# Optimization experiments

Hardware: AMD Instinct MI355X
Metric: run time of the kernel (lower is better)

The kernel has to match this reference:

```python
import jax, jax.numpy as jnp
import numpy as np

N_NODES = 100000
N_EDGES = 1600000
D = 128


def setup_inputs() -> dict:
    key = jax.random.key(0)
    ks = jax.random.split(key, 10)
    features = jax.random.normal(ks[0], (N_NODES, D), dtype=jnp.float32)
    edge_index = jax.random.randint(ks[1], (2, N_EDGES), 0, N_NODES, dtype=jnp.int64)
    edge_weight = jax.random.uniform(ks[2], (N_EDGES,), dtype=jnp.float32)
    scale = 1.0 / np.sqrt(D)
    W1 = jax.random.normal(ks[3], (D, D), dtype=jnp.float32) * scale
    b1 = jnp.zeros((D,), dtype=jnp.float32)
    a1 = jnp.full((D,), 0.25, dtype=jnp.float32)  # PReLU init
    W2 = jax.random.normal(ks[4], (D, D), dtype=jnp.float32) * scale
    b2 = jnp.zeros((D,), dtype=jnp.float32)
    a2 = jnp.full((D,), 0.25, dtype=jnp.float32)
    return {"features": features, "edge_index": edge_index, "edge_weight": edge_weight,
            "W1": W1, "b1": b1, "a1": a1, "W2": W2, "b2": b2, "a2": a2}


def _gcn_norm(edge_index, edge_weight, n_nodes):
    # PyG GCNConv default: add self-loops (weight 1), symmetric normalization.
    src, dst = edge_index[0], edge_index[1]
    loop = jnp.arange(n_nodes, dtype=src.dtype)
    src = jnp.concatenate([src, loop])
    dst = jnp.concatenate([dst, loop])
    w = jnp.concatenate([edge_weight, jnp.ones((n_nodes,), edge_weight.dtype)])
    deg = jax.ops.segment_sum(w, dst, num_segments=n_nodes)  # in-degree (target)
    dis = jnp.where(deg > 0, jax.lax.rsqrt(deg), 0.0)
    norm = dis[src] * w * dis[dst]  # [E + N]
    return src, dst, norm


def _gcn_layer(x, W, b, src, dst, norm, n_nodes):
    h = x @ W                                 # [N, D] dense GEMM first (PyG order)
    msg = h[src] * norm[:, None]              # gather + scale, [E+N, D]
    out = jax.ops.segment_sum(msg, dst, num_segments=n_nodes)
    return out + b


def _prelu(x, a):
    return jnp.where(x >= 0, x, a * x)


def reference(features, edge_index, edge_weight, W1, b1, a1, W2, b2, a2):
    n = features.shape[0]
    src, dst, norm = _gcn_norm(edge_index, edge_weight, n)
    # dropout is identity in eval mode
    x = _prelu(_gcn_layer(features, W1, b1, src, dst, norm, n), a1)
    x = _prelu(_gcn_layer(x, W2, b2, src, dst, norm, n), a2)
    return x
```

## Files before the change

### kernel.cpp

```cpp
#include <hip/hip_runtime.h>
#include <cstdint>

#define NN 100000
#define NE 1600000
#define DD 128
#define NB 250
#define BSZ 400

typedef unsigned int uint;
typedef unsigned short ushort;
typedef unsigned long long u64;

typedef __attribute__((ext_vector_type(8))) short short8;
typedef __attribute__((ext_vector_type(4))) float floatx4;

__device__ inline uint f2bf(float f) {
    uint u = __float_as_uint(f);
    return (u + 0x7fffu + ((u >> 16) & 1u)) >> 16;
}


__global__ __launch_bounds__(256) void zero_bc(uint* __restrict__ bc) {
    if (threadIdx.x < NB) bc[threadIdx.x] = 0u;
}

__global__ __launch_bounds__(256) void bucket_hist(const int* __restrict__ dst,
                                                   uint* __restrict__ bc) {
    __shared__ uint h[NB];
    int tid = threadIdx.x;
    if (tid < NB) h[tid] = 0u;
    __syncthreads();
    int e0 = blockIdx.x * 8192 + tid;
#pragma unroll
    for (int k = 0; k < 32; ++k) {
        int e = e0 + 256 * k;
        if (e < NE) atomicAdd(&h[(uint)dst[e] / BSZ], 1u);
    }
    __syncthreads();
    if (tid < NB && h[tid]) atomicAdd(&bc[tid], h[tid]);
}

__global__ __launch_bounds__(256) void bucket_prefix(const uint* __restrict__ bc,
                                                     uint* __restrict__ bbase,
                                                     uint* __restrict__ bcur) {
    int lane = threadIdx.x;
    if (lane < 64) {
        uint v[4], s = 0;
#pragma unroll
        for (int k = 0; k < 4; ++k) {
            int i = lane * 4 + k;
            v[k] = (i < NB) ? bc[i] : 0u;
            s += v[k];
        }
        uint inc = s;
#pragma unroll
        for (int d = 1; d < 64; d <<= 1) {
            uint t = __shfl_up(inc, (unsigned)d, 64);
            if (lane >= d) inc += t;
        }
        uint run = inc - s;
#pragma unroll
        for (int k = 0; k < 4; ++k) {
            int i = lane * 4 + k;
            if (i < NB) { bbase[i] = run; bcur[i] = run; run += v[k]; }
        }
        if (lane == 63) bbase[NB] = run;
    }
}

__global__ __launch_bounds__(256) void bucket_append(const int* __restrict__ src,
                                                     const int* __restrict__ dst,
                                                     const float* __restrict__ w,
                                                     uint* __restrict__ bcur,
                                                     int2* __restrict__ etmp) {
    __shared__ uint h[NB];
    __shared__ uint res[NB];
    int tid = threadIdx.x;
    if (tid < NB) h[tid] = 0u;
    __syncthreads();
    int e0 = blockIdx.x * 4096 + tid;
    uint rank[16], bkt[16];
#pragma unroll
    for (int k = 0; k < 16; ++k) {
        int e = e0 + 256 * k;
        if (e < NE) {
            uint b = (uint)dst[e] / BSZ;
            bkt[k] = b;
            rank[k] = atomicAdd(&h[b], 1u);
        } else bkt[k] = 0xffffffffu;
    }
    __syncthreads();
    if (tid < NB) res[tid] = h[tid] ? atomicAdd(&bcur[tid], h[tid]) : 0u;
    __syncthreads();
#pragma unroll
    for (int k = 0; k < 16; ++k) {
        if (bkt[k] != 0xffffffffu) {
            int e = e0 + 256 * k;
            uint dl = (uint)dst[e] - bkt[k] * BSZ;
            uint wq = (uint)(w[e] * 8388608.0f);
            if (wq > 8388607u) wq = 8388607u;
            etmp[res[bkt[k]] + rank[k]] = make_int2(src[e], (int)((dl << 23) | wq));
        }
    }
}

__global__ __launch_bounds__(256) void bucket_build(const int2* __restrict__ etmp,
                                                    const uint* __restrict__ bbase,
                                                    float* __restrict__ dis,
                                                    int* __restrict__ hist_g,
                                                    int* __restrict__ rowstart,
                                                    int2* __restrict__ edges) {
    __shared__ u64   wc[BSZ];
    __shared__ uint  cur[BSZ];
    __shared__ float disl[BSZ];
    int tid = threadIdx.x;
    int b = blockIdx.x;
    int n0 = b * BSZ;
    for (int i = tid; i < BSZ; i += 256) wc[i] = 0ull;
    __syncthreads();
    uint base = bbase[b], end = bbase[b + 1];
    for (uint i = base + tid; i < end; i += 256) {
        uint y = (uint)etmp[i].y;
        uint dl = y >> 23;
        atomicAdd(&wc[dl], ((u64)1 << 40) | (u64)(y & 0x7fffffu));
    }
    __syncthreads();
    if (tid < 64) {
        uint v[7], s = 0;
#pragma unroll
        for (int k = 0; k < 7; ++k) {
            int i = tid * 7 + k;
            v[k] = (i < BSZ) ? (uint)(wc[i] >> 40) : 0u;
            s += v[k];
        }
        uint inc = s;
#pragma unroll
        for (int d = 1; d < 64; d <<= 1) {
            uint t = __shfl_up(inc, (unsigned)d, 64);
            if (tid >= d) inc += t;
        }
        uint run = inc - s;
#pragma unroll
        for (int k = 0; k < 7; ++k) {
            int i = tid * 7 + k;
            if (i < BSZ) { cur[i] = run; run += v[k]; }
        }
    }
    __syncthreads();
    for (int i = tid; i < BSZ; i += 256) {
        u64 v = wc[i];
        float wsum = (float)(v & 0xffffffffffull) * (1.0f / 8388608.0f);
        float ds = rsqrtf(1.0f + wsum);
        disl[i] = ds;
        dis[n0 + i] = ds;
        hist_g[n0 + i] = (int)(v >> 40);
        rowstart[n0 + i] = (int)(base + cur[i]);
    }
    __syncthreads();
    for (uint i = base + tid; i < end; i += 256) {
        int2 e = etmp[i];
        uint y = (uint)e.y;
        uint dl = y >> 23;
        float wv = (float)(y & 0x7fffffu) * (1.0f / 8388608.0f);
        uint p = atomicAdd(&cur[dl], 1u);
        float nrm = wv * disl[dl];
        edges[base + p] = make_int2(e.x, __float_as_int(nrm));
    }
}

#define WTS 136
#define NTILES ((NN + 63) / 64)

template <bool AF32>
__global__ __launch_bounds__(256) void gemm_mfma(const void* __restrict__ Xv,
                                                 const float* __restrict__ W,
                                                 const float* __restrict__ dis,
                                                 ushort* __restrict__ HB) {
    __shared__ ushort Wt[DD * WTS];
    int tid = threadIdx.x;
#pragma unroll
    for (int it = 0; it < 16; ++it) {
        int flat = (tid + it * 256) * 4;
        int k = flat >> 7, n = flat & 127;
        float4 wv = *(const float4*)&W[flat];
        Wt[(n + 0) * WTS + k] = (ushort)f2bf(wv.x);
        Wt[(n + 1) * WTS + k] = (ushort)f2bf(wv.y);
        Wt[(n + 2) * WTS + k] = (ushort)f2bf(wv.z);
        Wt[(n + 3) * WTS + k] = (ushort)f2bf(wv.w);
    }
    __syncthreads();

    int wave = tid >> 6, lane = tid & 63;
    int q = lane >> 4, l16 = lane & 15;

    for (int tile = blockIdx.x; tile < NTILES; tile += gridDim.x) {
        int row0 = tile * 64 + wave * 16;

        int arow = row0 + l16;
        if (arow >= NN) arow = NN - 1;
        short8 afr[4];
        if (AF32) {
            const float* xr = (const float*)Xv + (size_t)arow * DD + q * 8;
#pragma unroll
            for (int ks = 0; ks < 4; ++ks) {
                float4 f0 = *(const float4*)(xr + ks * 32);
                float4 f1 = *(const float4*)(xr + ks * 32 + 4);
                uint4 u;
                u.x = f2bf(f0.x) | (f2bf(f0.y) << 16);
                u.y = f2bf(f0.z) | (f2bf(f0.w) << 16);
                u.z = f2bf(f1.x) | (f2bf(f1.y) << 16);
                u.w = f2bf(f1.z) | (f2bf(f1.w) << 16);
                afr[ks] = __builtin_bit_cast(short8, u);
            }
        } else {
            const ushort* xr = (const ushort*)Xv + (size_t)arow * DD + q * 8;
#pragma unroll
            for (int ks = 0; ks < 4; ++ks)
                afr[ks] = *(const short8*)(xr + ks * 32);
        }

        floatx4 acc[8];
#pragma unroll
        for (int ct = 0; ct < 8; ++ct) acc[ct] = (floatx4)(0.0f);

#pragma unroll
        for (int ct = 0; ct < 8; ++ct) {
            const ushort* wp = &Wt[(ct * 16 + l16) * WTS + q * 8];
#pragma unroll
            for (int ks = 0; ks < 4; ++ks) {
                short8 bfr = *(const short8*)(wp + ks * 32);
                acc[ct] = __builtin_amdgcn_mfma_f32_16x16x32_bf16(afr[ks], bfr, acc[ct], 0, 0, 0);
            }
        }

#pragma unroll
        for (int reg = 0; reg < 4; ++reg) {
            int r = row0 + q * 4 + reg;
            if (r < NN) {
                float ds = dis[r];
                ushort* orow = HB + (size_t)r * DD + l16;
#pragma unroll
                for (int ct = 0; ct < 8; ++ct)
                    orow[ct * 16] = (ushort)f2bf(acc[ct][reg] * ds);
            }
        }
    }
}

template <bool BF16OUT>
__global__ __launch_bounds__(256) void gather_finalize(const ushort* __restrict__ hb,
                                                       const int2* __restrict__ edges,
                                                       const int* __restrict__ rowstart,
                                                       const int* __restrict__ hist,
                                                       const float* __restrict__ dis,
                                                       const float* __restrict__ b,
                                                       const float* __restrict__ a,
                                                       void* __restrict__ xout) {
    int wid = __builtin_amdgcn_readfirstlane(threadIdx.x >> 6);
    int lane = threadIdx.x & 63;
    int node = blockIdx.x * 4 + wid;
    uint lane4 = (uint)lane * 4u;

    int rs  = rowstart[node];
    int cnt = hist[node];
    float ds = dis[node];
    const int2* ep = edges + rs;
    const char* hbase = (const char*)hb;

    uint su = *(const uint*)(hbase + ((uint)node << 8) + lane4);
    float2 acc0, acc1, acc2, acc3;
    acc0.x = __uint_as_float(su << 16) * ds;
    acc0.y = __uint_as_float(su & 0xffff0000u) * ds;
    acc1 = make_float2(0.f, 0.f);
    acc2 = make_float2(0.f, 0.f);
    acc3 = make_float2(0.f, 0.f);

    int full = cnt >> 4;
    int t = 0;
    for (; t < full; ++t) {
        int2 e[16];
#pragma unroll
        for (int k = 0; k < 16; ++k) e[k] = ep[t * 16 + k];
#pragma unroll
        for (int k = 0; k < 16; ++k) {
            uint voff = ((uint)e[k].x << 8) + lane4;
            uint g = *(const uint*)(hbase + voff);
            float nrm = __int_as_float(e[k].y);
            float2* ac = (k & 3) == 0 ? &acc0 : (k & 3) == 1 ? &acc1 : (k & 3) == 2 ? &acc2 : &acc3;
            ac->x += __uint_as_float(g << 16) * nrm;
            ac->y += __uint_as_float(g & 0xffff0000u) * nrm;
        }
    }
    int remn = cnt & 15;
    if (remn) {
        int2 e[16];
#pragma unroll
        for (int k = 0; k < 16; ++k) e[k] = ep[t * 16 + k];
#pragma unroll
        for (int k = 0; k < 16; ++k) {
            bool live = k < remn;
            uint sidx = live ? (uint)e[k].x : 0u;
            float nrm = live ? __int_as_float(e[k].y) : 0.0f;
            uint voff = (sidx << 8) + lane4;
            uint g = *(const uint*)(hbase + voff);
            float2* ac = (k & 3) == 0 ? &acc0 : (k & 3) == 1 ? &acc1 : (k & 3) == 2 ? &acc2 : &acc3;
            ac->x += __uint_as_float(g << 16) * nrm;
            ac->y += __uint_as_float(g & 0xffff0000u) * nrm;
        }
    }

    float2 bb = ((const float2*)b)[lane];
    float2 aa = ((const float2*)a)[lane];
    float r0 = acc0.x + acc1.x + acc2.x + acc3.x + bb.x;
    float r1 = acc0.y + acc1.y + acc2.y + acc3.y + bb.y;
    r0 = r0 >= 0.f ? r0 : aa.x * r0;
    r1 = r1 >= 0.f ? r1 : aa.y * r1;
    if (BF16OUT) {
        ((uint*)xout)[(size_t)node * 64 + lane] = f2bf(r0) | (f2bf(r1) << 16);
    } else {
        float2 o; o.x = r0; o.y = r1;
        ((float2*)xout)[(size_t)node * 64 + lane] = o;
    }
}

extern "C" void kernel_launch(void* const* d_in, const int* in_sizes, int n_in,
                              void* d_out, int out_size, void* d_ws, size_t ws_size,
                              hipStream_t stream) {
    const float* feat = (const float*)d_in[0];
    const int*   ei   = (const int*)d_in[1];
    const float* ew   = (const float*)d_in[2];
    const float* W1   = (const float*)d_in[3];
    const float* b1   = (const float*)d_in[4];
    const float* a1   = (const float*)d_in[5];
    const float* W2   = (const float*)d_in[6];
    const float* b2   = (const float*)d_in[7];
    const float* a2   = (const float*)d_in[8];
    float* out = (float*)d_out;

    const int* srcp = ei;
    const int* dstp = ei + NE;

    char* wsb = (char*)d_ws;
    size_t off = 0;
    uint* bc     = (uint*)(wsb + off); off += 4096;
    uint* bbase  = (uint*)(wsb + off); off += 4096;
    uint* bcur   = (uint*)(wsb + off); off += 4096;
    float* dis   = (float*)(wsb + off); off += 4ull * NN;
    int* hist    = (int*)(wsb + off); off += 4ull * NN;
    int* rowstart= (int*)(wsb + off); off += 4ull * NN;
    int2* etmp   = (int2*)(wsb + off); off += 8ull * NE;
    int2* edges  = (int2*)(wsb + off); off += 8ull * NE;
    ushort* hb   = (ushort*)(wsb + off); off += 2ull * NN * DD;
    ushort* x1b  = (ushort*)(wsb + off); off += 2ull * NN * DD;

    zero_bc<<<1, 256, 0, stream>>>(bc);
    bucket_hist<<<(NE + 8191) / 8192, 256, 0, stream>>>(dstp, bc);
    bucket_prefix<<<1, 256, 0, stream>>>(bc, bbase, bcur);
    bucket_append<<<(NE + 4095) / 4096, 256, 0, stream>>>(srcp, dstp, ew, bcur, etmp);
    bucket_build<<<NB, 256, 0, stream>>>(etmp, bbase, dis, hist, rowstart, edges);

    const int gemm_blocks = (NTILES + 1) / 2;
    const int gath_blocks = NN / 4;

    gemm_mfma<true><<<gemm_blocks, 256, 0, stream>>>(feat, W1, dis, hb);
    gather_finalize<true><<<gath_blocks, 256, 0, stream>>>(hb, edges, rowstart, hist, dis, b1, a1, x1b);
    gemm_mfma<false><<<gemm_blocks, 256, 0, stream>>>(x1b, W2, dis, hb);
    gather_finalize<false><<<gath_blocks, 256, 0, stream>>>(hb, edges, rowstart, hist, dis, b2, a2, out);
}
```

Before: 364.8 us.

## Remove zero kernel, precompute bf16 weights once, widen bucket_build blocks

New measurement: 343.9 us. -5.7%, faster.

```diff
diff --git a/kernel.cpp b/kernel.cpp
--- a/kernel.cpp
+++ b/kernel.cpp
@@ -6,6 +6,7 @@
 #define DD 128
 #define NB 250
 #define BSZ 400
+#define NHB ((NE + 8191) / 8192)
 
 typedef unsigned int uint;
 typedef unsigned short ushort;
@@ -19,15 +20,20 @@
     return (u + 0x7fffu + ((u >> 16) & 1u)) >> 16;
 }
 
-
-__global__ __launch_bounds__(256) void zero_bc(uint* __restrict__ bc) {
-    if (threadIdx.x < NB) bc[threadIdx.x] = 0u;
-}
-
 __global__ __launch_bounds__(256) void bucket_hist(const int* __restrict__ dst,
-                                                   uint* __restrict__ bc) {
+                                                   uint* __restrict__ bcp,
+                                                   const float* __restrict__ W1,
+                                                   const float* __restrict__ W2,
+                                                   ushort* __restrict__ Wt1,
+                                                   ushort* __restrict__ Wt2) {
     __shared__ uint h[NB];
     int tid = threadIdx.x;
+    int gi = blockIdx.x * 256 + tid;
+    if (gi < DD * DD) {
+        int k = gi >> 7, n = gi & 127;
+        Wt1[n * DD + k] = (ushort)f2bf(W1[gi]);
+        Wt2[n * DD + k] = (ushort)f2bf(W2[gi]);
+    }
     if (tid < NB) h[tid] = 0u;
     __syncthreads();
     int e0 = blockIdx.x * 8192 + tid;
@@ -37,19 +43,32 @@
         if (e < NE) atomicAdd(&h[(uint)dst[e] / BSZ], 1u);
     }
     __syncthreads();
-    if (tid < NB && h[tid]) atomicAdd(&bc[tid], h[tid]);
-}
-
-__global__ __launch_bounds__(256) void bucket_prefix(const uint* __restrict__ bc,
+    if (tid < NB) bcp[(size_t)tid * NHB + blockIdx.x] = h[tid];
+}
+
+__global__ __launch_bounds__(256) void bucket_prefix(const uint* __restrict__ bcp,
                                                      uint* __restrict__ bbase,
                                                      uint* __restrict__ bcur) {
-    int lane = threadIdx.x;
+    __shared__ uint cnt[NB];
+    int tid = threadIdx.x;
+    if (tid < NB) {
+        const uint4* p = (const uint4*)(bcp + (size_t)tid * NHB);
+        uint s = 0;
+#pragma unroll 7
+        for (int j = 0; j < NHB / 4; ++j) {
+            uint4 v = p[j];
+            s += v.x + v.y + v.z + v.w;
+        }
+        cnt[tid] = s;
+    }
+    __syncthreads();
+    int lane = tid;
     if (lane < 64) {
         uint v[4], s = 0;
 #pragma unroll
         for (int k = 0; k < 4; ++k) {
             int i = lane * 4 + k;
-            v[k] = (i < NB) ? bc[i] : 0u;
+            v[k] = (i < NB) ? cnt[i] : 0u;
             s += v[k];
         }
         uint inc = s;
@@ -104,22 +123,22 @@
     }
 }
 
-__global__ __launch_bounds__(256) void bucket_build(const int2* __restrict__ etmp,
-                                                    const uint* __restrict__ bbase,
-                                                    float* __restrict__ dis,
-                                                    int* __restrict__ hist_g,
-                                                    int* __restrict__ rowstart,
-                                                    int2* __restrict__ edges) {
+__global__ __launch_bounds__(1024) void bucket_build(const int2* __restrict__ etmp,
+                                                     const uint* __restrict__ bbase,
+                                                     float* __restrict__ dis,
+                                                     int* __restrict__ hist_g,
+                                                     int* __restrict__ rowstart,
+                                                     int2* __restrict__ edges) {
     __shared__ u64   wc[BSZ];
     __shared__ uint  cur[BSZ];
     __shared__ float disl[BSZ];
     int tid = threadIdx.x;
     int b = blockIdx.x;
     int n0 = b * BSZ;
-    for (int i = tid; i < BSZ; i += 256) wc[i] = 0ull;
+    for (int i = tid; i < BSZ; i += 1024) wc[i] = 0ull;
     __syncthreads();
     uint base = bbase[b], end = bbase[b + 1];
-    for (uint i = base + tid; i < end; i += 256) {
+    for (uint i = base + tid; i < end; i += 1024) {
         uint y = (uint)etmp[i].y;
         uint dl = y >> 23;
         atomicAdd(&wc[dl], ((u64)1 << 40) | (u64)(y & 0x7fffffu));
@@ -147,7 +166,7 @@
         }
     }
     __syncthreads();
-    for (int i = tid; i < BSZ; i += 256) {
+    for (int i = tid; i < BSZ; i += 1024) {
         u64 v = wc[i];
         float wsum = (float)(v & 0xffffffffffull) * (1.0f / 8388608.0f);
         float ds = rsqrtf(1.0f + wsum);
@@ -157,7 +176,7 @@
         rowstart[n0 + i] = (int)(base + cur[i]);
     }
     __syncthreads();
-    for (uint i = base + tid; i < end; i += 256) {
+    for (uint i = base + tid; i < end; i += 1024) {
         int2 e = etmp[i];
         uint y = (uint)e.y;
         uint dl = y >> 23;
@@ -173,20 +192,17 @@
 
 template <bool AF32>
 __global__ __launch_bounds__(256) void gemm_mfma(const void* __restrict__ Xv,
-                                                 const float* __restrict__ W,
+                                                 const ushort* __restrict__ Wtg,
                                                  const float* __restrict__ dis,
                                                  ushort* __restrict__ HB) {
     __shared__ ushort Wt[DD * WTS];
     int tid = threadIdx.x;
 #pragma unroll
-    for (int it = 0; it < 16; ++it) {
-        int flat = (tid + it * 256) * 4;
-        int k = flat >> 7, n = flat & 127;
-        float4 wv = *(const float4*)&W[flat];
-        Wt[(n + 0) * WTS + k] = (ushort)f2bf(wv.x);
-        Wt[(n + 1) * WTS + k] = (ushort)f2bf(wv.y);
-        Wt[(n + 2) * WTS + k] = (ushort)f2bf(wv.z);
-        Wt[(n + 3) * WTS + k] = (ushort)f2bf(wv.w);
+    for (int u = 0; u < 8; ++u) {
+        int unit = tid + u * 256;
+        int n = unit >> 4, c = unit & 15;
+        short8 v = *(const short8*)(Wtg + n * DD + c * 8);
+        *(short8*)&Wt[n * WTS + c * 8] = v;
     }
     __syncthreads();
 
@@ -267,7 +283,7 @@
     const int2* ep = edges + rs;
     const char* hbase = (const char*)hb;
 
-    uint su = *(const uint*)(hbase + ((uint)node << 8) + lane4);
+    uint su = *(const uint*)(hbase + ((size_t)(uint)node << 8) + lane4);
     float2 acc0, acc1, acc2, acc3;
     acc0.x = __uint_as_float(su << 16) * ds;
     acc0.y = __uint_as_float(su & 0xffff0000u) * ds;
@@ -284,7 +300,7 @@
 #pragma unroll
         for (int k = 0; k < 16; ++k) {
             uint voff = ((uint)e[k].x << 8) + lane4;
-            uint g = *(const uint*)(hbase + voff);
+            uint g = *(const uint*)(hbase + (size_t)voff);
             float nrm = __int_as_float(e[k].y);
             float2* ac = (k & 3) == 0 ? &acc0 : (k & 3) == 1 ? &acc1 : (k & 3) == 2 ? &acc2 : &acc3;
             ac->x += __uint_as_float(g << 16) * nrm;
@@ -302,7 +318,7 @@
             uint sidx = live ? (uint)e[k].x : 0u;
             float nrm = live ? __int_as_float(e[k].y) : 0.0f;
             uint voff = (sidx << 8) + lane4;
-            uint g = *(const uint*)(hbase + voff);
+            uint g = *(const uint*)(hbase + (size_t)voff);
             float2* ac = (k & 3) == 0 ? &acc0 : (k & 3) == 1 ? &acc1 : (k & 3) == 2 ? &acc2 : &acc3;
             ac->x += __uint_as_float(g << 16) * nrm;
             ac->y += __uint_as_float(g & 0xffff0000u) * nrm;
@@ -342,7 +358,9 @@
 
     char* wsb = (char*)d_ws;
     size_t off = 0;
-    uint* bc     = (uint*)(wsb + off); off += 4096;
+    uint* bcp    = (uint*)(wsb + off); off += 262144;
+    ushort* wt1  = (ushort*)(wsb + off); off += 2ull * DD * DD;
+    ushort* wt2  = (ushort*)(wsb + off); off += 2ull * DD * DD;
     uint* bbase  = (uint*)(wsb + off); off += 4096;
     uint* bcur   = (uint*)(wsb + off); off += 4096;
     float* dis   = (float*)(wsb + off); off += 4ull * NN;
@@ -353,17 +371,16 @@
     ushort* hb   = (ushort*)(wsb + off); off += 2ull * NN * DD;
     ushort* x1b  = (ushort*)(wsb + off); off += 2ull * NN * DD;
 
-    zero_bc<<<1, 256, 0, stream>>>(bc);
-    bucket_hist<<<(NE + 8191) / 8192, 256, 0, stream>>>(dstp, bc);
-    bucket_prefix<<<1, 256, 0, stream>>>(bc, bbase, bcur);
+    bucket_hist<<<NHB, 256, 0, stream>>>(dstp, bcp, W1, W2, wt1, wt2);
+    bucket_prefix<<<1, 256, 0, stream>>>(bcp, bbase, bcur);
     bucket_append<<<(NE + 4095) / 4096, 256, 0, stream>>>(srcp, dstp, ew, bcur, etmp);
-    bucket_build<<<NB, 256, 0, stream>>>(etmp, bbase, dis, hist, rowstart, edges);
+    bucket_build<<<NB, 1024, 0, stream>>>(etmp, bbase, dis, hist, rowstart, edges);
 
     const int gemm_blocks = (NTILES + 1) / 2;
     const int gath_blocks = NN / 4;
 
-    gemm_mfma<true><<<gemm_blocks, 256, 0, stream>>>(feat, W1, dis, hb);
+    gemm_mfma<true><<<gemm_blocks, 256, 0, stream>>>(feat, wt1, dis, hb);
     gather_finalize<true><<<gath_blocks, 256, 0, stream>>>(hb, edges, rowstart, hist, dis, b1, a1, x1b);
-    gemm_mfma<false><<<gemm_blocks, 256, 0, stream>>>(x1b, W2, dis, hb);
+    gemm_mfma<false><<<gemm_blocks, 256, 0, stream>>>(x1b, wt2, dis, hb);
     gather_finalize<false><<<gath_blocks, 256, 0, stream>>>(hb, edges, rowstart, hist, dis, b2, a2, out);
 }
```
